# Kernel tuning notes

Measured on AMD Instinct MI355X. Metric: run time of the kernel, lower is better.

## Reference

```python
import jax, jax.numpy as jnp
import numpy as np

SCALE = 8  # window size (scale[0])

def setup_inputs() -> dict:
    key = jax.random.key(0)
    kx, kw, kb = jax.random.split(key, 3)
    B, T, D = 1, 16384, 512
    x = jax.random.normal(kx, (B, T, D), dtype=jnp.float32)
    # fc = Linear(SCALE*D -> D) stored as [in, out] for x @ W + b
    W = jax.random.normal(kw, (SCALE * D, D), dtype=jnp.float32) / np.sqrt(SCALE * D)
    b = jax.random.normal(kb, (D,), dtype=jnp.float32) * 0.01
    return {"x": x, "W": W, "b": b}

def _windows(x):
    """Faithful sliding-window extraction matching the torch loop:
    start=max(0,i-3), end=min(i+4,T), segment=x[:,start:end+1], right-padded to SCALE."""
    B, T, D = x.shape
    i = jnp.arange(T)
    start = jnp.maximum(0, i - SCALE // 2 + 1)            # [T]
    end = jnp.minimum(i + SCALE // 2, T)                  # [T]
    L = jnp.minimum(end + 1, T) - start                   # actual segment length
    j = jnp.arange(SCALE)
    # positions past the segment map to index T -> a zero pad row
    idx = jnp.where(j[None, :] < L[:, None], start[:, None] + j[None, :], T)  # [T, SCALE]
    xp = jnp.concatenate([x, jnp.zeros((B, 1, D), x.dtype)], axis=1)          # [B, T+1, D]
    return xp[:, idx, :]                                   # [B, T, SCALE, D]

def reference(x, W, b):
    B, T, D = x.shape
    win = _windows(x)                                      # [B, T, S, D]
    wfft = jnp.fft.fft(win, axis=2).real.astype(x.dtype)   # real part of FFT over window
    coarse = wfft.mean(axis=2)                             # [B, T, D]
    fine = wfft.reshape(B, T, SCALE * D)                   # [B, T, S*D]
    fine = jax.nn.gelu(fine @ W + b, approximate=False)    # Linear + exact GELU (torch default)
    return coarse, fine
```

## Files before the change

kernel.cpp:

```cpp
#include <hip/hip_runtime.h>
#include <math.h>

#define T_LEN 16384
#define DDIM  512
#define PADR  8
#define XROWS (T_LEN + 64)
#define BM 128
#define BN 128
#define SLAB 160

typedef unsigned short u16;
typedef __attribute__((ext_vector_type(4))) float  f32x4;
typedef __attribute__((ext_vector_type(8))) __bf16 bf16x8;
typedef __attribute__((ext_vector_type(8))) unsigned short u16x8;
typedef __attribute__((ext_vector_type(4))) unsigned short u16x4;

__device__ __forceinline__ float bf2f(u16 h) {
  return __uint_as_float(((unsigned)h) << 16);
}
__device__ __forceinline__ u16 f2bf(float f) {
  unsigned u = __float_as_uint(f);
  return (u16)((u + 0x7fffu + ((u >> 16) & 1u)) >> 16);
}
__device__ __forceinline__ float gelu_exact(float v) {
  return 0.5f * v * (1.0f + erff(v * 0.7071067811865475f));
}
__device__ __forceinline__ void gll16(const void* g, void* l) {
  __builtin_amdgcn_global_load_lds(
      (const __attribute__((address_space(1))) void*)g,
      (__attribute__((address_space(3))) void*)l, 16, 0, 0);
}

__device__ const float g_C[8] = {1.0f, 0.70710678118654752f, 0.0f, -0.70710678118654752f,
                                 -1.0f, -0.70710678118654752f, 0.0f, 0.70710678118654752f};

__global__ __launch_bounds__(256) void k_fold(const float* __restrict__ W, u16* __restrict__ wt) {
  __shared__ u16 tile[64][65];
  int kd0 = blockIdx.x * 64;
  int n0  = blockIdx.y * 64;
  int j   = kd0 >> 9;
  int d0  = kd0 & 511;
  int t   = threadIdx.x;
  int nl  = t & 63;
  int dseg = t >> 6;
  for (int s = 0; s < 16; ++s) {
    int dl = dseg * 16 + s;
    float acc = 0.f;
#pragma unroll
    for (int k = 0; k < 8; ++k)
      acc += g_C[(j * k) & 7] * W[(size_t)(k * 512 + d0 + dl) * 512 + n0 + nl];
    tile[dl][nl] = f2bf(acc);
  }
  __syncthreads();
  int r  = t >> 2;
  int c0 = (t & 3) * 16;
  u16* dst = wt + (size_t)(n0 + r) * 4096 + kd0 + c0;
  u16x8 v0, v1;
#pragma unroll
  for (int u = 0; u < 8; ++u) { v0[u] = tile[c0 + u][r]; v1[u] = tile[c0 + 8 + u][r]; }
  *(u16x8*)dst = v0;
  *(u16x8*)(dst + 8) = v1;
}

__global__ __launch_bounds__(256) void k_prep(const float* __restrict__ x,
                                              u16* __restrict__ xpad,
                                              float* __restrict__ outc) {
  int bid = blockIdx.x;
  if (bid >= 8192) {
    int z = (bid - 8192) * 256 + threadIdx.x;
    u16x8 zero = {};
    if (z < 512) {
      *(u16x8*)&xpad[(size_t)z * 8] = zero;
    } else {
      size_t zz = (size_t)(z - 512);
      *(u16x8*)&xpad[(size_t)(PADR + T_LEN) * 512 + zz * 8] = zero;
    }
    return;
  }
  long t = (long)bid * 256 + threadIdx.x;
  long idx = t * 4;
  int i = (int)(idx >> 9);
  int d = (int)(idx & 511);
  f32x4 v = *(const f32x4*)&x[idx];
  u16x4 o;
#pragma unroll
  for (int u = 0; u < 4; ++u) o[u] = f2bf(v[u]);
  *(u16x4*)&xpad[(size_t)(i + PADR) * 512 + d] = o;
  if (i <= T_LEN - 4) *(f32x4*)&outc[(size_t)(i + 3) * 512 + d] = v;
  if (i == 0) {
    *(f32x4*)&outc[(size_t)0 * 512 + d] = v;
    *(f32x4*)&outc[(size_t)1 * 512 + d] = v;
    *(f32x4*)&outc[(size_t)2 * 512 + d] = v;
  }
}

__global__ __launch_bounds__(256, 2) void k_gemm(const u16* __restrict__ xpad,
                                                 const u16* __restrict__ wt,
                                                 const float* __restrict__ bias,
                                                 float* __restrict__ fine) {
  __shared__ __align__(16) u16 As[SLAB * 64];
  __shared__ __align__(16) u16 Bs[BN * 64];
  int n0 = blockIdx.x * BN;
  int i0 = blockIdx.y * BM;
  int t = threadIdx.x;
  int lane = t & 63;
  int wid = t >> 6;
  int wr = wid >> 1, wc = wid & 1;
  f32x4 acc[4][4] = {};

  for (int kc = 0; kc < 8; ++kc) {
#pragma unroll
    for (int p = 0; p < 5; ++p) {
      int off = p * 4096 + t * 16;
      int row = off >> 7;
      int slot = (off >> 4) & 7;
      const u16* src = xpad + (size_t)(i0 + 5 + row) * 512 + kc * 64 + slot * 8;
      gll16(src, (char*)As + off);
    }
    for (int jo = 0; jo < 8; ++jo) {
#pragma unroll
      for (int p = 0; p < 4; ++p) {
        int off = p * 4096 + t * 16;
        int nr = off >> 7;
        int slot = (off >> 4) & 7;
        const u16* src = wt + (size_t)(n0 + nr) * 4096 + jo * 512 + kc * 64 + slot * 8;
        gll16(src, (char*)Bs + off);
      }
      __syncthreads();
      int arow = wr * 64 + (lane & 15) + jo;
      int brow = wc * 64 + (lane & 15);
      int kb = (lane >> 4) * 8;
#pragma unroll
      for (int ks = 0; ks < 2; ++ks) {
        bf16x8 a[4], b[4];
#pragma unroll
        for (int mi = 0; mi < 4; ++mi)
          a[mi] = *(const bf16x8*)&As[(arow + mi * 16) * 64 + ks * 32 + kb];
#pragma unroll
        for (int ni = 0; ni < 4; ++ni)
          b[ni] = *(const bf16x8*)&Bs[(brow + ni * 16) * 64 + ks * 32 + kb];
#pragma unroll
        for (int mi = 0; mi < 4; ++mi)
#pragma unroll
          for (int ni = 0; ni < 4; ++ni)
            acc[mi][ni] = __builtin_amdgcn_mfma_f32_16x16x32_bf16(a[mi], b[ni], acc[mi][ni], 0, 0, 0);
      }
      __syncthreads();
    }
  }
#pragma unroll
  for (int ni = 0; ni < 4; ++ni) {
    int n = n0 + wc * 64 + ni * 16 + (lane & 15);
    float bv = bias[n];
#pragma unroll
    for (int mi = 0; mi < 4; ++mi) {
      int ib = i0 + wr * 64 + mi * 16 + ((lane >> 4) * 4);
      f32x4 v = acc[mi][ni];
#pragma unroll
      for (int e = 0; e < 4; ++e)
        fine[(size_t)(ib + e) * 512 + n] = gelu_exact(v[e] + bv);
    }
  }
}

__global__ __launch_bounds__(256) void k_edge(const u16* __restrict__ xpad, const u16* __restrict__ wt,
                                              const float* __restrict__ bias, float* __restrict__ fine) {
  int o = blockIdx.x * 4 + (threadIdx.x >> 6);
  int lane = threadIdx.x & 63;
  int i = o >> 9;
  int n = o & 511;
  int len = (i + 5) * 512;
  const u16* xr = xpad + PADR * 512;
  const u16* wrow = wt + (size_t)n * 4096;
  float s = 0.f;
#pragma unroll
  for (int m = 0; m < 7; ++m) {
    int k = (m * 64 + lane) * 8;
    if (k < len) {
      u16x8 xv = *(const u16x8*)&xr[k];
      u16x8 wv = *(const u16x8*)&wrow[k];
#pragma unroll
      for (int u = 0; u < 8; ++u) s += bf2f(xv[u]) * bf2f(wv[u]);
    }
  }
#pragma unroll
  for (int off = 32; off; off >>= 1) s += __shfl_xor(s, off);
  if (lane == 0) fine[(size_t)i * 512 + n] = gelu_exact(s + bias[n]);
}

extern "C" void kernel_launch(void* const* d_in, const int* in_sizes, int n_in,
                              void* d_out, int out_size, void* d_ws, size_t ws_size,
                              hipStream_t stream) {
  const float* x = (const float*)d_in[0];
  const float* W = (const float*)d_in[1];
  const float* b = (const float*)d_in[2];
  float* outc = (float*)d_out;
  float* outf = (float*)d_out + (size_t)T_LEN * DDIM;

  u16* xpad = (u16*)d_ws;
  u16* wt   = (u16*)((char*)d_ws + (size_t)XROWS * 512 * 2);

  k_fold <<<dim3(64, 8),   256, 0, stream>>>(W, wt);
  k_prep <<<dim3(8208),    256, 0, stream>>>(x, xpad, outc);
  k_gemm <<<dim3(4, 128),  256, 0, stream>>>(xpad, wt, b, outf);
  k_edge <<<dim3(384),     256, 0, stream>>>(xpad, wt, b, outf);
}
```

Baseline: 212.3 us.

## Rewrite GEMM as triple-buffered 256x128 tile pipeline with swizzled LDS

Replaces the GEMM kernel with a 512-thread, 256x128 tile version. It walks the full K=4096 dimension in 64-wide steps and triple-buffers the A and B tiles in LDS, loading them asynchronously with global_load_lds. An XOR slot swizzle is meant to avoid LDS bank conflicts. Staging of the next tiles is interleaved with MFMA phases under explicit barriers, waitcnt and setprio, and a block-id remap is added for cache locality. The cost removed is serialized load-then-compute stalls; in exchange it drops the old reuse of one A slab across the eight window offsets, and its large LDS footprint limits occupancy to one block per CU with 256 blocks.

Result: faster. 189.4 us (-10.8%).

```diff
diff --git a/kernel.cpp b/kernel.cpp
--- a/kernel.cpp
+++ b/kernel.cpp
@@ -5,9 +5,11 @@
 #define DDIM  512
 #define PADR  8
 #define XROWS (T_LEN + 64)
-#define BM 128
+#define BM 256
 #define BN 128
-#define SLAB 160
+#define AELEMS 16384
+#define BELEMS 8192
+#define BUFELEMS (AELEMS + BELEMS)
 
 typedef unsigned short u16;
 typedef __attribute__((ext_vector_type(4))) float  f32x4;
@@ -94,71 +96,134 @@
   }
 }
 
-__global__ __launch_bounds__(256, 2) void k_gemm(const u16* __restrict__ xpad,
+
+__device__ __forceinline__ void stageA(const u16* __restrict__ xpad, u16* dstA,
+                                       int i0, int k0, int tid, int p) {
+  int c = p * 512 + tid;
+  int r = c >> 3;
+  int sl = (c & 7) ^ (r & 7);
+  gll16(xpad + (size_t)(i0 + 5 + r) * 512 + k0 + sl * 8, dstA + (size_t)c * 8);
+}
+__device__ __forceinline__ void stageB(const u16* __restrict__ wt, u16* dstB,
+                                       int n0, int k0, int tid, int p) {
+  int c = p * 512 + tid;
+  int r = c >> 3;
+  int sl = (c & 7) ^ (r & 7);
+  gll16(wt + (size_t)(n0 + r) * 4096 + k0 + sl * 8, dstB + (size_t)c * 8);
+}
+__device__ __forceinline__ bf16x8 rdfrag(const u16* base, int row, int slot_log) {
+  int sl = slot_log ^ (row & 7);
+  return *(const bf16x8*)(base + row * 64 + sl * 8);
+}
+
+#define MFMA __builtin_amdgcn_mfma_f32_16x16x32_bf16
+
+template<int MODE>
+__device__ __forceinline__ void kstep(const u16* __restrict__ xpad, const u16* __restrict__ wt,
+                                      const u16* Ab, const u16* Bb, u16* An, u16* Bn,
+                                      int i0, int n0, int k0n, int tid, int lane, int wr, int wc,
+                                      f32x4 (&acc)[8][2]) {
+  int slg = lane >> 4;
+  int br = wc * 32 + (lane & 15);
+  bf16x8 b00 = rdfrag(Bb, br, slg);
+  bf16x8 b01 = rdfrag(Bb, br, slg + 4);
+  bf16x8 b10 = rdfrag(Bb, br + 16, slg);
+  bf16x8 b11 = rdfrag(Bb, br + 16, slg + 4);
+
+#define PHASE(MQ, STG, TAIL)                                                  \
+  {                                                                           \
+    int ar = wr * 128 + (MQ) * 32 + (lane & 15);                              \
+    bf16x8 a00 = rdfrag(Ab, ar, slg);                                         \
+    bf16x8 a01 = rdfrag(Ab, ar, slg + 4);                                     \
+    bf16x8 a10 = rdfrag(Ab, ar + 16, slg);                                    \
+    bf16x8 a11 = rdfrag(Ab, ar + 16, slg + 4);                                \
+    STG                                                                       \
+    __builtin_amdgcn_s_barrier();                                             \
+    asm volatile("s_waitcnt lgkmcnt(0)" ::: "memory");                        \
+    __builtin_amdgcn_sched_barrier(0);                                        \
+    __builtin_amdgcn_s_setprio(1);                                            \
+    acc[(MQ)*2][0]   = MFMA(a00, b00, acc[(MQ)*2][0],   0, 0, 0);             \
+    acc[(MQ)*2][0]   = MFMA(a01, b01, acc[(MQ)*2][0],   0, 0, 0);             \
+    acc[(MQ)*2][1]   = MFMA(a00, b10, acc[(MQ)*2][1],   0, 0, 0);             \
+    acc[(MQ)*2][1]   = MFMA(a01, b11, acc[(MQ)*2][1],   0, 0, 0);             \
+    acc[(MQ)*2+1][0] = MFMA(a10, b00, acc[(MQ)*2+1][0], 0, 0, 0);             \
+    acc[(MQ)*2+1][0] = MFMA(a11, b01, acc[(MQ)*2+1][0], 0, 0, 0);             \
+    acc[(MQ)*2+1][1] = MFMA(a10, b10, acc[(MQ)*2+1][1], 0, 0, 0);             \
+    acc[(MQ)*2+1][1] = MFMA(a11, b11, acc[(MQ)*2+1][1], 0, 0, 0);             \
+    __builtin_amdgcn_s_setprio(0);                                            \
+    TAIL                                                                      \
+    __builtin_amdgcn_s_barrier();                                             \
+  }
+
+  if constexpr (MODE == 0) {
+    PHASE(0, { stageA(xpad, An, i0, k0n, tid, 0); stageA(xpad, An, i0, k0n, tid, 1); }, {})
+    PHASE(1, { stageA(xpad, An, i0, k0n, tid, 2); stageA(xpad, An, i0, k0n, tid, 3); }, {})
+    PHASE(2, { stageB(wt, Bn, n0, k0n, tid, 0);   stageB(wt, Bn, n0, k0n, tid, 1);   }, {})
+    PHASE(3, {}, { asm volatile("s_waitcnt vmcnt(6)" ::: "memory"); })
+  } else if constexpr (MODE == 1) {
+    PHASE(0, {}, {})
+    PHASE(1, {}, {})
+    PHASE(2, {}, {})
+    PHASE(3, {}, { asm volatile("s_waitcnt vmcnt(0)" ::: "memory"); })
+  } else {
+    PHASE(0, {}, {})
+    PHASE(1, {}, {})
+    PHASE(2, {}, {})
+    PHASE(3, {}, {})
+  }
+#undef PHASE
+}
+
+__global__ __launch_bounds__(512, 2) void k_gemm(const u16* __restrict__ xpad,
                                                  const u16* __restrict__ wt,
                                                  const float* __restrict__ bias,
                                                  float* __restrict__ fine) {
-  __shared__ __align__(16) u16 As[SLAB * 64];
-  __shared__ __align__(16) u16 Bs[BN * 64];
-  int n0 = blockIdx.x * BN;
-  int i0 = blockIdx.y * BM;
-  int t = threadIdx.x;
-  int lane = t & 63;
-  int wid = t >> 6;
-  int wr = wid >> 1, wc = wid & 1;
-  f32x4 acc[4][4] = {};
-
-  for (int kc = 0; kc < 8; ++kc) {
-#pragma unroll
-    for (int p = 0; p < 5; ++p) {
-      int off = p * 4096 + t * 16;
-      int row = off >> 7;
-      int slot = (off >> 4) & 7;
-      const u16* src = xpad + (size_t)(i0 + 5 + row) * 512 + kc * 64 + slot * 8;
-      gll16(src, (char*)As + off);
-    }
-    for (int jo = 0; jo < 8; ++jo) {
-#pragma unroll
-      for (int p = 0; p < 4; ++p) {
-        int off = p * 4096 + t * 16;
-        int nr = off >> 7;
-        int slot = (off >> 4) & 7;
-        const u16* src = wt + (size_t)(n0 + nr) * 4096 + jo * 512 + kc * 64 + slot * 8;
-        gll16(src, (char*)Bs + off);
-      }
-      __syncthreads();
-      int arow = wr * 64 + (lane & 15) + jo;
-      int brow = wc * 64 + (lane & 15);
-      int kb = (lane >> 4) * 8;
-#pragma unroll
-      for (int ks = 0; ks < 2; ++ks) {
-        bf16x8 a[4], b[4];
-#pragma unroll
-        for (int mi = 0; mi < 4; ++mi)
-          a[mi] = *(const bf16x8*)&As[(arow + mi * 16) * 64 + ks * 32 + kb];
-#pragma unroll
-        for (int ni = 0; ni < 4; ++ni)
-          b[ni] = *(const bf16x8*)&Bs[(brow + ni * 16) * 64 + ks * 32 + kb];
-#pragma unroll
-        for (int mi = 0; mi < 4; ++mi)
-#pragma unroll
-          for (int ni = 0; ni < 4; ++ni)
-            acc[mi][ni] = __builtin_amdgcn_mfma_f32_16x16x32_bf16(a[mi], b[ni], acc[mi][ni], 0, 0, 0);
-      }
-      __syncthreads();
-    }
-  }
-#pragma unroll
-  for (int ni = 0; ni < 4; ++ni) {
-    int n = n0 + wc * 64 + ni * 16 + (lane & 15);
-    float bv = bias[n];
-#pragma unroll
-    for (int mi = 0; mi < 4; ++mi) {
-      int ib = i0 + wr * 64 + mi * 16 + ((lane >> 4) * 4);
-      f32x4 v = acc[mi][ni];
+  __shared__ __align__(16) u16 lds[3][BUFELEMS];
+  int orig = blockIdx.x;
+  int id = (orig & 7) * 32 + (orig >> 3);
+  int n0 = (id & 3) * BN;
+  int i0 = (id >> 2) * BM;
+  int tid = threadIdx.x;
+  int lane = tid & 63;
+  int wid = tid >> 6;
+  int wr = wid >> 2, wc = wid & 3;
+  f32x4 acc[8][2] = {};
+
+#pragma unroll
+  for (int p = 0; p < 4; ++p) stageA(xpad, &lds[0][0], i0, 0, tid, p);
+#pragma unroll
+  for (int p = 0; p < 2; ++p) stageB(wt, &lds[0][AELEMS], n0, 0, tid, p);
+#pragma unroll
+  for (int p = 0; p < 4; ++p) stageA(xpad, &lds[1][0], i0, 64, tid, p);
+#pragma unroll
+  for (int p = 0; p < 2; ++p) stageB(wt, &lds[1][AELEMS], n0, 64, tid, p);
+  asm volatile("s_waitcnt vmcnt(6)" ::: "memory");
+  __builtin_amdgcn_s_barrier();
+
+  int b = 0;
+  for (int t = 0; t < 62; ++t) {
+    int bs = b + 2; if (bs >= 3) bs -= 3;
+    kstep<0>(xpad, wt, &lds[b][0], &lds[b][AELEMS], &lds[bs][0], &lds[bs][AELEMS],
+             i0, n0, (t + 2) * 64, tid, lane, wr, wc, acc);
+    if (++b == 3) b = 0;
+  }
+  kstep<1>(xpad, wt, &lds[b][0], &lds[b][AELEMS], nullptr, nullptr,
+           i0, n0, 0, tid, lane, wr, wc, acc);
+  if (++b == 3) b = 0;
+  kstep<2>(xpad, wt, &lds[b][0], &lds[b][AELEMS], nullptr, nullptr,
+           i0, n0, 0, tid, lane, wr, wc, acc);
+
+#pragma unroll
+  for (int n = 0; n < 2; ++n) {
+    int col = n0 + wc * 32 + n * 16 + (lane & 15);
+    float bv = bias[col];
+#pragma unroll
+    for (int m = 0; m < 8; ++m) {
+      int row = i0 + wr * 128 + m * 16 + ((lane >> 4) * 4);
+      f32x4 v = acc[m][n];
 #pragma unroll
       for (int e = 0; e < 4; ++e)
-        fine[(size_t)(ib + e) * 512 + n] = gelu_exact(v[e] + bv);
+        fine[(size_t)(row + e) * 512 + col] = gelu_exact(v[e] + bv);
     }
   }
 }
@@ -202,6 +267,6 @@
 
   k_fold <<<dim3(64, 8),   256, 0, stream>>>(W, wt);
   k_prep <<<dim3(8208),    256, 0, stream>>>(x, xpad, outc);
-  k_gemm <<<dim3(4, 128),  256, 0, stream>>>(xpad, wt, b, outf);
+  k_gemm <<<dim3(256),     512, 0, stream>>>(xpad, wt, b, outf);
   k_edge <<<dim3(384),     256, 0, stream>>>(xpad, wt, b, outf);
 }
```

## Pipeline GEMM with double-buffered A, quad-buffered B, swizzled LDS and larger tiles

Applied to the files above, without the earlier changes.

The GEMM is rewritten around a software pipeline. The A slab is double-buffered across k-chunks and B tiles sit in a 4-deep ring, with global-to-LDS loads issued ahead and fenced by explicit vmcnt waits and barriers. The M tile grows to 256 rows with 512 threads, LDS slots are XOR-swizzled to avoid bank conflicts, and blocks are remapped for L2 locality. The aim is to hide memory latency behind MFMA work and cut LDS conflicts. In exchange it uses much more LDS, which may limit occupancy, and the hand-tuned waitcnt counts are fragile.

After: 176.6 us. 16.8% less time.

```diff
diff --git a/kernel.cpp b/kernel.cpp
--- a/kernel.cpp
+++ b/kernel.cpp
@@ -5,9 +5,11 @@
 #define DDIM  512
 #define PADR  8
 #define XROWS (T_LEN + 64)
-#define BM 128
+#define BM 256
 #define BN 128
-#define SLAB 160
+#define SLABR 320
+#define AELEMS (SLABR * 64)
+#define BELEMS 8192
 
 typedef unsigned short u16;
 typedef __attribute__((ext_vector_type(4))) float  f32x4;
@@ -94,71 +96,153 @@
   }
 }
 
-__global__ __launch_bounds__(256, 2) void k_gemm(const u16* __restrict__ xpad,
+
+__device__ __forceinline__ void stageA(const u16* __restrict__ xpad, u16* dstA,
+                                       int i0, int colbase, int tid, int p) {
+  int c = p * 512 + tid;
+  int r = c >> 3;
+  int sl = (c & 7) ^ (r & 7);
+  gll16(xpad + (size_t)(i0 + 5 + r) * 512 + colbase + sl * 8, dstA + (size_t)c * 8);
+}
+__device__ __forceinline__ void stageB(const u16* __restrict__ wt, u16* dstB,
+                                       int n0, int colbase, int tid, int p) {
+  int c = p * 512 + tid;
+  int r = c >> 3;
+  int sl = (c & 7) ^ (r & 7);
+  gll16(wt + (size_t)(n0 + r) * 4096 + colbase + sl * 8, dstB + (size_t)c * 8);
+}
+__device__ __forceinline__ bf16x8 rdfrag(const u16* base, int row, int slot_log) {
+  int sl = slot_log ^ (row & 7);
+  return *(const bf16x8*)(base + row * 64 + sl * 8);
+}
+
+#define MFMA __builtin_amdgcn_mfma_f32_16x16x32_bf16
+
+template<int NT>
+__device__ __forceinline__ void vwait() {
+  if constexpr (NT == 0)      asm volatile("s_waitcnt vmcnt(0)" ::: "memory");
+  else if constexpr (NT == 2) asm volatile("s_waitcnt vmcnt(2)" ::: "memory");
+  else if constexpr (NT == 3) asm volatile("s_waitcnt vmcnt(3)" ::: "memory");
+  else if constexpr (NT == 4) asm volatile("s_waitcnt vmcnt(4)" ::: "memory");
+}
+
+template<int S, bool APASS, bool BSTG, int NTAIL, bool DOWAIT>
+__device__ __forceinline__ void gstep(const u16* __restrict__ xpad, const u16* __restrict__ wt,
+                                      const u16* Ac, u16* An, u16* Bbase,
+                                      int i0, int n0, int kc, int lane, int wr, int wc,
+                                      int tid, f32x4 (&acc)[4][4]) {
+  const u16* Br = Bbase + (size_t)(S & 3) * BELEMS;
+  u16* Bw = Bbase + (size_t)((S + 2) & 3) * BELEMS;
+  int slg = lane >> 4;
+  int abase = wr * 64 + (lane & 15) + S;
+  int bbase = wc * 64 + (lane & 15);
+
+  {
+    bf16x8 a[4], b[4];
+#pragma unroll
+    for (int m = 0; m < 4; ++m) a[m] = rdfrag(Ac, abase + m * 16, slg);
+#pragma unroll
+    for (int n = 0; n < 4; ++n) b[n] = rdfrag(Br, bbase + n * 16, slg);
+    if constexpr (BSTG) {
+      int colB = ((S + 2) & 7) * 512 + (kc + ((S + 2) >> 3)) * 64;
+      stageB(wt, Bw, n0, colB, tid, 0);
+      stageB(wt, Bw, n0, colB, tid, 1);
+    }
+    __builtin_amdgcn_s_barrier();
+    asm volatile("s_waitcnt lgkmcnt(0)" ::: "memory");
+    __builtin_amdgcn_sched_barrier(0);
+    __builtin_amdgcn_s_setprio(1);
+#pragma unroll
+    for (int m = 0; m < 4; ++m)
+#pragma unroll
+      for (int n = 0; n < 4; ++n)
+        acc[m][n] = MFMA(a[m], b[n], acc[m][n], 0, 0, 0);
+    __builtin_amdgcn_s_setprio(0);
+    __builtin_amdgcn_s_barrier();
+  }
+  {
+    bf16x8 a[4], b[4];
+#pragma unroll
+    for (int m = 0; m < 4; ++m) a[m] = rdfrag(Ac, abase + m * 16, slg + 4);
+#pragma unroll
+    for (int n = 0; n < 4; ++n) b[n] = rdfrag(Br, bbase + n * 16, slg + 4);
+    if constexpr (APASS) stageA(xpad, An, i0, (kc + 1) * 64, tid, S);
+    __builtin_amdgcn_s_barrier();
+    asm volatile("s_waitcnt lgkmcnt(0)" ::: "memory");
+    __builtin_amdgcn_sched_barrier(0);
+    __builtin_amdgcn_s_setprio(1);
+#pragma unroll
+    for (int m = 0; m < 4; ++m)
+#pragma unroll
+      for (int n = 0; n < 4; ++n)
+        acc[m][n] = MFMA(a[m], b[n], acc[m][n], 0, 0, 0);
+    __builtin_amdgcn_s_setprio(0);
+    if constexpr (DOWAIT) vwait<NTAIL>();
+    __builtin_amdgcn_s_barrier();
+  }
+}
+
+__global__ __launch_bounds__(512, 2) void k_gemm(const u16* __restrict__ xpad,
                                                  const u16* __restrict__ wt,
                                                  const float* __restrict__ bias,
                                                  float* __restrict__ fine) {
-  __shared__ __align__(16) u16 As[SLAB * 64];
-  __shared__ __align__(16) u16 Bs[BN * 64];
-  int n0 = blockIdx.x * BN;
-  int i0 = blockIdx.y * BM;
-  int t = threadIdx.x;
-  int lane = t & 63;
-  int wid = t >> 6;
+  __shared__ __align__(16) u16 lds[2 * AELEMS + 4 * BELEMS];
+  int orig = blockIdx.x;
+  int id = (orig & 7) * 32 + (orig >> 3);
+  int n0 = (id & 3) * BN;
+  int i0 = (id >> 2) * BM;
+  int tid = threadIdx.x;
+  int lane = tid & 63;
+  int wid = tid >> 6;
   int wr = wid >> 1, wc = wid & 1;
   f32x4 acc[4][4] = {};
 
-  for (int kc = 0; kc < 8; ++kc) {
-#pragma unroll
-    for (int p = 0; p < 5; ++p) {
-      int off = p * 4096 + t * 16;
-      int row = off >> 7;
-      int slot = (off >> 4) & 7;
-      const u16* src = xpad + (size_t)(i0 + 5 + row) * 512 + kc * 64 + slot * 8;
-      gll16(src, (char*)As + off);
-    }
-    for (int jo = 0; jo < 8; ++jo) {
-#pragma unroll
-      for (int p = 0; p < 4; ++p) {
-        int off = p * 4096 + t * 16;
-        int nr = off >> 7;
-        int slot = (off >> 4) & 7;
-        const u16* src = wt + (size_t)(n0 + nr) * 4096 + jo * 512 + kc * 64 + slot * 8;
-        gll16(src, (char*)Bs + off);
-      }
-      __syncthreads();
-      int arow = wr * 64 + (lane & 15) + jo;
-      int brow = wc * 64 + (lane & 15);
-      int kb = (lane >> 4) * 8;
-#pragma unroll
-      for (int ks = 0; ks < 2; ++ks) {
-        bf16x8 a[4], b[4];
-#pragma unroll
-        for (int mi = 0; mi < 4; ++mi)
-          a[mi] = *(const bf16x8*)&As[(arow + mi * 16) * 64 + ks * 32 + kb];
-#pragma unroll
-        for (int ni = 0; ni < 4; ++ni)
-          b[ni] = *(const bf16x8*)&Bs[(brow + ni * 16) * 64 + ks * 32 + kb];
-#pragma unroll
-        for (int mi = 0; mi < 4; ++mi)
-#pragma unroll
-          for (int ni = 0; ni < 4; ++ni)
-            acc[mi][ni] = __builtin_amdgcn_mfma_f32_16x16x32_bf16(a[mi], b[ni], acc[mi][ni], 0, 0, 0);
-      }
-      __syncthreads();
-    }
-  }
-#pragma unroll
-  for (int ni = 0; ni < 4; ++ni) {
-    int n = n0 + wc * 64 + ni * 16 + (lane & 15);
-    float bv = bias[n];
-#pragma unroll
-    for (int mi = 0; mi < 4; ++mi) {
-      int ib = i0 + wr * 64 + mi * 16 + ((lane >> 4) * 4);
-      f32x4 v = acc[mi][ni];
+  u16* A0 = &lds[0];
+  u16* A1 = &lds[AELEMS];
+  u16* Bb = &lds[2 * AELEMS];
+
+#pragma unroll
+  for (int p = 0; p < 5; ++p) stageA(xpad, A0, i0, 0, tid, p);
+  stageB(wt, Bb, n0, 0, tid, 0);
+  stageB(wt, Bb, n0, 0, tid, 1);
+  stageB(wt, Bb + BELEMS, n0, 512, tid, 0);
+  stageB(wt, Bb + BELEMS, n0, 512, tid, 1);
+  asm volatile("s_waitcnt vmcnt(2)" ::: "memory");
+  __builtin_amdgcn_s_barrier();
+
+  u16* Ac = A0;
+  u16* An = A1;
+  for (int kc = 0; kc < 7; ++kc) {
+    gstep<0, true,  true, 3, true>(xpad, wt, Ac, An, Bb, i0, n0, kc, lane, wr, wc, tid, acc);
+    gstep<1, true,  true, 4, true>(xpad, wt, Ac, An, Bb, i0, n0, kc, lane, wr, wc, tid, acc);
+    gstep<2, true,  true, 4, true>(xpad, wt, Ac, An, Bb, i0, n0, kc, lane, wr, wc, tid, acc);
+    gstep<3, true,  true, 4, true>(xpad, wt, Ac, An, Bb, i0, n0, kc, lane, wr, wc, tid, acc);
+    gstep<4, true,  true, 4, true>(xpad, wt, Ac, An, Bb, i0, n0, kc, lane, wr, wc, tid, acc);
+    gstep<5, false, true, 3, true>(xpad, wt, Ac, An, Bb, i0, n0, kc, lane, wr, wc, tid, acc);
+    gstep<6, false, true, 2, true>(xpad, wt, Ac, An, Bb, i0, n0, kc, lane, wr, wc, tid, acc);
+    gstep<7, false, true, 2, true>(xpad, wt, Ac, An, Bb, i0, n0, kc, lane, wr, wc, tid, acc);
+    u16* tmp = Ac; Ac = An; An = tmp;
+  }
+  gstep<0, false, true,  2, true >(xpad, wt, Ac, An, Bb, i0, n0, 7, lane, wr, wc, tid, acc);
+  gstep<1, false, true,  2, true >(xpad, wt, Ac, An, Bb, i0, n0, 7, lane, wr, wc, tid, acc);
+  gstep<2, false, true,  2, true >(xpad, wt, Ac, An, Bb, i0, n0, 7, lane, wr, wc, tid, acc);
+  gstep<3, false, true,  2, true >(xpad, wt, Ac, An, Bb, i0, n0, 7, lane, wr, wc, tid, acc);
+  gstep<4, false, true,  2, true >(xpad, wt, Ac, An, Bb, i0, n0, 7, lane, wr, wc, tid, acc);
+  gstep<5, false, true,  2, true >(xpad, wt, Ac, An, Bb, i0, n0, 7, lane, wr, wc, tid, acc);
+  gstep<6, false, false, 0, true >(xpad, wt, Ac, An, Bb, i0, n0, 7, lane, wr, wc, tid, acc);
+  gstep<7, false, false, 0, false>(xpad, wt, Ac, An, Bb, i0, n0, 7, lane, wr, wc, tid, acc);
+
+#pragma unroll
+  for (int n = 0; n < 4; ++n) {
+    int col = n0 + wc * 64 + n * 16 + (lane & 15);
+    float bv = bias[col];
+#pragma unroll
+    for (int m = 0; m < 4; ++m) {
+      int row = i0 + wr * 64 + m * 16 + ((lane >> 4) * 4);
+      f32x4 v = acc[m][n];
 #pragma unroll
       for (int e = 0; e < 4; ++e)
-        fine[(size_t)(ib + e) * 512 + n] = gelu_exact(v[e] + bv);
+        fine[(size_t)(row + e) * 512 + col] = gelu_exact(v[e] + bv);
     }
   }
 }
@@ -202,6 +286,6 @@
 
   k_fold <<<dim3(64, 8),   256, 0, stream>>>(W, wt);
   k_prep <<<dim3(8208),    256, 0, stream>>>(x, xpad, outc);
-  k_gemm <<<dim3(4, 128),  256, 0, stream>>>(xpad, wt, b, outf);
+  k_gemm <<<dim3(256),     512, 0, stream>>>(xpad, wt, b, outf);
   k_edge <<<dim3(384),     256, 0, stream>>>(xpad, wt, b, outf);
 }
```
